# Performance work log

Measured on AMD Instinct MI355X. Metric: run time of the kernel, lower is better.

Reference implementation:

```python
import jax, jax.numpy as jnp
import numpy as np

ALPHA = 0.2  # LeakyReLU negative slope
NEG_INF = -9e15


def _gat_layer(Wh, adj, a, concat):
    """One GraphAttentionLayer given pre-projected Wh [B,N,F].
    Algebraic split of the concat attention: e[b,i,j] = lrelu(Wh[i]@a1 + Wh[j]@a2),
    identical math to matmul(cat(Wh_i, Wh_j), a)."""
    F_ = Wh.shape[-1]
    f1 = Wh @ a[:F_, 0]   # [B,N]
    f2 = Wh @ a[F_:, 0]   # [B,N]
    e = jax.nn.leaky_relu(f1[:, :, None] + f2[:, None, :], negative_slope=ALPHA)  # [B,N,N]
    e = jnp.where(adj > 0, e, NEG_INF)
    att = jax.nn.softmax(e, axis=-1)            # dropout omitted (eval mode)
    h_prime = jnp.einsum('bij,bjf->bif', att, Wh)
    return jax.nn.elu(h_prime) if concat else h_prime


def setup_inputs() -> dict:
    key = jax.random.key(0)
    ks = jax.random.split(key, 9)
    B, N, Fin, H, nH, Fout = 4, 2048, 512, 128, 4, 256
    x = jax.random.normal(ks[0], (B, N, Fin), dtype=jnp.float32)
    adj = jax.random.randint(ks[1], (B, N, N), 0, 2, dtype=jnp.int32)
    mask = jnp.ones((B, N), dtype=jnp.float32)
    s = 0.05
    W_heads = jax.random.normal(ks[2], (nH, Fin, H), dtype=jnp.float32) * s
    a_heads = jax.random.normal(ks[3], (nH, 2 * H, 1), dtype=jnp.float32) * s
    W_out = jax.random.normal(ks[4], (nH * H, Fout), dtype=jnp.float32) * s
    a_out = jax.random.normal(ks[5], (2 * Fout, 1), dtype=jnp.float32) * s
    W_pool = jax.random.normal(ks[6], (Fout, Fout), dtype=jnp.float32) * s
    b_pool = jax.random.normal(ks[7], (Fout,), dtype=jnp.float32) * s
    return {"x": x, "adj": adj, "mask": mask, "W_heads": W_heads, "a_heads": a_heads,
            "W_out": W_out, "a_out": a_out, "W_pool": W_pool, "b_pool": b_pool}


def reference(x, adj, mask, W_heads, a_heads, W_out, a_out, W_pool, b_pool):
    # multi-head GAT layer, heads concatenated (dropout = identity in eval)
    heads = [_gat_layer(x @ W_heads[h], adj, a_heads[h], concat=True)
             for h in range(W_heads.shape[0])]
    xcat = jnp.concatenate(heads, axis=-1)                 # [B,N,nH*H]
    x_out = _gat_layer(xcat @ W_out, adj, a_out, concat=False)  # [B,N,Fout]
    x_out = x_out * mask[:, :, None]
    pooled = x_out.sum(axis=1) / (mask.sum(axis=1, keepdims=True) + 1e-10)
    graph_embedding = jax.nn.relu(pooled @ W_pool + b_pool)
    return graph_embedding, x_out
```

## Files before the change

kernel.cpp:

```cpp
#include <hip/hip_runtime.h>

typedef unsigned short u16;
typedef __attribute__((ext_vector_type(8))) short s8v;
typedef __attribute__((ext_vector_type(8))) unsigned short us8;
typedef __attribute__((ext_vector_type(4))) float f4v;

#define L2E 1.4426950408889634f

typedef __attribute__((address_space(1))) void gvoid_t;
typedef __attribute__((address_space(3))) void lvoid_t;

__device__ __forceinline__ u16 f2bf(float f) {
  unsigned u = __builtin_bit_cast(unsigned, f);
  return (u16)((u + 0x7FFFu + ((u >> 16) & 1u)) >> 16);
}
__device__ __forceinline__ float bf2f(u16 h) {
  return __builtin_bit_cast(float, ((unsigned)h) << 16);
}
__device__ __forceinline__ f4v mfma16(s8v a, s8v b, f4v c) {
  return __builtin_amdgcn_mfma_f32_16x16x32_bf16(a, b, c, 0, 0, 0);
}
__device__ __forceinline__ float exp2fast(float x) {
#if __has_builtin(__builtin_amdgcn_exp2f)
  return __builtin_amdgcn_exp2f(x);
#else
  return exp2f(x);
#endif
}
__device__ __forceinline__ void stage16(const u16* g, u16* lds_arr, int slot) {
#if __has_builtin(__builtin_amdgcn_global_load_lds)
  __builtin_amdgcn_global_load_lds((gvoid_t*)(g),
      (lvoid_t*)(lds_arr + (size_t)(slot & ~63) * 8), 16, 0, 0);
#else
  *(us8*)(lds_arr + (size_t)slot * 8) = *(const us8*)g;
#endif
}

__global__ __launch_bounds__(256) void prep_x(const float* __restrict__ x,
                                              u16* __restrict__ xb) {
  int i = (blockIdx.x * 256 + threadIdx.x) * 8;
  float4 v0 = *(const float4*)(x + i);
  float4 v1 = *(const float4*)(x + i + 4);
  us8 o;
  o[0] = f2bf(v0.x); o[1] = f2bf(v0.y); o[2] = f2bf(v0.z); o[3] = f2bf(v0.w);
  o[4] = f2bf(v1.x); o[5] = f2bf(v1.y); o[6] = f2bf(v1.z); o[7] = f2bf(v1.w);
  *(us8*)(xb + i) = o;
}

__global__ __launch_bounds__(256) void prep_wall(const float* __restrict__ W,
                                                 u16* __restrict__ Wt) {
  int idx = blockIdx.x * 256 + threadIdx.x;
  int h = idx >> 16, k = (idx >> 7) & 511, f = idx & 127;
  Wt[(size_t)(h * 128 + f) * 512 + k] = f2bf(W[idx]);
}
__global__ __launch_bounds__(256) void prep_wout(const float* __restrict__ W,
                                                 u16* __restrict__ Wt) {
  int idx = blockIdx.x * 256 + threadIdx.x;
  int k = idx >> 8, c = idx & 255;
  Wt[(size_t)c * 512 + k] = f2bf(W[idx]);
}
__global__ __launch_bounds__(256) void prep_adj(const int* __restrict__ adj,
                                                unsigned* __restrict__ adjw) {
  int chunk = blockIdx.x * 4 + (threadIdx.x >> 6);
  int l = threadIdx.x & 63;
  int v = adj[(size_t)chunk * 64 + l];
  unsigned long long m = __ballot(v != 0);
  if (l == 0) {
    ((uint2*)adjw)[chunk] = make_uint2((unsigned)m, (unsigned)(m >> 32));
  }
}

__global__ __launch_bounds__(256) void gemm_bf16(const u16* __restrict__ A,
                                                 const u16* __restrict__ Bt,
                                                 u16* __restrict__ Ct, int CO) {
  const int K = 512, N = 2048;
  int m0 = blockIdx.x * 128;
  int n0 = blockIdx.y * 128;
  int t = threadIdx.x;
  int w = t >> 6, l = t & 63, lr = l & 15, lq = l >> 4;
  int wr = w >> 1, wc = w & 1;
  __shared__ u16 As[2][128 * 32];
  __shared__ u16 Bs[2][128 * 32];
  f4v zero4 = {0.f, 0.f, 0.f, 0.f};
  f4v acc[4][4];
#pragma unroll
  for (int i = 0; i < 4; ++i)
#pragma unroll
    for (int j = 0; j < 4; ++j) acc[i][j] = zero4;

  auto stage = [&](int buf, int kt) {
    int k0 = kt * 32;
    int row = t >> 2, ch = t & 3;
    int q = (ch ^ ((row >> 1) & 3)) * 8;
    stage16(A + (size_t)(m0 + row) * K + k0 + q, As[buf], t);
    stage16(Bt + (size_t)(n0 + row) * K + k0 + q, Bs[buf], t);
    int s2 = t + 256;
    row = s2 >> 2; ch = s2 & 3;
    q = (ch ^ ((row >> 1) & 3)) * 8;
    stage16(A + (size_t)(m0 + row) * K + k0 + q, As[buf], s2);
    stage16(Bt + (size_t)(n0 + row) * K + k0 + q, Bs[buf], s2);
  };
  stage(0, 0);
  int swz = (lq ^ ((lr >> 1) & 3)) * 8;
  for (int kt = 0; kt < 16; ++kt) {
    __syncthreads();
    if (kt < 15) stage((kt + 1) & 1, kt + 1);
    const u16* as = As[kt & 1];
    const u16* bs = Bs[kt & 1];
    s8v af[4], bfr[4];
#pragma unroll
    for (int rf = 0; rf < 4; ++rf)
      af[rf] = *(const s8v*)&as[(wr * 64 + rf * 16 + lr) * 32 + swz];
#pragma unroll
    for (int nf = 0; nf < 4; ++nf)
      bfr[nf] = *(const s8v*)&bs[(wc * 64 + nf * 16 + lr) * 32 + swz];
#pragma unroll
    for (int rf = 0; rf < 4; ++rf)
#pragma unroll
      for (int nf = 0; nf < 4; ++nf)
        acc[rf][nf] = mfma16(af[rf], bfr[nf], acc[rf][nf]);
  }
  int bidx = m0 >> 11;
  int nr0 = m0 & 2047;
#pragma unroll
  for (int rf = 0; rf < 4; ++rf) {
#pragma unroll
    for (int nf = 0; nf < 4; ++nf) {
      int col = n0 + wc * 64 + nf * 16 + lr;
      int nr = nr0 + wr * 64 + rf * 16 + lq * 4;
      f4v a = acc[rf][nf];
      ushort4 v = make_ushort4(f2bf(a[0]), f2bf(a[1]), f2bf(a[2]), f2bf(a[3]));
      *(ushort4*)&Ct[((size_t)bidx * CO + col) * N + nr] = v;
    }
  }
}

__global__ __launch_bounds__(256) void fkern(const u16* __restrict__ Wht,
                                             const float* __restrict__ a,
                                             float* __restrict__ f1L,
                                             float* __restrict__ f2L, int COLS,
                                             int F) {
  const int N = 2048;
  int h = blockIdx.z, b = blockIdx.y;
  int nl = threadIdx.x & 63, fc = threadIdx.x >> 6;
  int n = blockIdx.x * 64 + nl;
  int F4 = F >> 2;
  const u16* colp = Wht + ((size_t)(b * COLS + h * F + fc * F4)) * N + n;
  const float* ah = a + h * 2 * F + fc * F4;
  float a1 = 0.f, a2 = 0.f;
  for (int c = 0; c < F4; ++c) {
    float v = bf2f(colp[(size_t)c * N]);
    a1 = fmaf(v, ah[c], a1);
    a2 = fmaf(v, ah[F + c], a2);
  }
  __shared__ float r1[4][64], r2[4][64];
  r1[fc][nl] = a1;
  r2[fc][nl] = a2;
  __syncthreads();
  if (fc == 0) {
    float s1 = r1[0][nl] + r1[1][nl] + r1[2][nl] + r1[3][nl];
    float s2 = r2[0][nl] + r2[1][nl] + r2[2][nl] + r2[3][nl];
    f1L[(size_t)(h * 4 + b) * N + n] = s1 * L2E;
    f2L[(size_t)(h * 4 + b) * N + n] = s2 * L2E;
  }
}

__global__ __launch_bounds__(256) void fmax_kern(const float* __restrict__ f2L,
                                                 float* __restrict__ f2m) {
  int row = blockIdx.x;
  const float* p = f2L + (size_t)row * 2048;
  int t = threadIdx.x;
  float v = -__builtin_inff();
  for (int k = 0; k < 8; ++k) v = fmaxf(v, p[t + k * 256]);
#pragma unroll
  for (int d = 1; d < 64; d <<= 1) v = fmaxf(v, __shfl_xor(v, d));
  __shared__ float wm[4];
  if ((t & 63) == 0) wm[t >> 6] = v;
  __syncthreads();
  if (t == 0) f2m[row] = fmaxf(fmaxf(wm[0], wm[1]), fmaxf(wm[2], wm[3]));
}

template <int CT, int WR, bool ELU>
__global__ __launch_bounds__(256, 2) void attn_kernel(
    const u16* __restrict__ Wht, const float* __restrict__ f1L,
    const float* __restrict__ f2L, const float* __restrict__ f2max,
    const unsigned* __restrict__ adjw, const float* __restrict__ mask,
    void* __restrict__ outp) {
  const int N = 2048;
  constexpr int WC = 4 / WR;
  constexpr int NF = 8 / WC;
  constexpr int NCH = CT / 128;
  constexpr int ROWS = WR * 16;
  constexpr int NT = 2048 / ROWS;
  constexpr int FHD = (CT == 512) ? 1 : 0;
  int kb = blockIdx.x;
  int x = kb & 7, g = kb >> 3;
  int p = x + 8 * (g / NT);
  int it = g % NT;
  int b = p / NCH, ch = p % NCH;
  int i0 = it * ROWS, col0 = ch * 128;
  int fh = FHD ? ch : 0;
  int t = threadIdx.x;
  int w = t >> 6, l = t & 63, lr = l & 15, lq = l >> 4;
  int wc = w & (WC - 1), wrs = w / WC;

  __shared__ u16 Vs[2][128 * 64];
  __shared__ unsigned adjs[ROWS * 65];
  __shared__ float f2s[2048];

  const float* f1p = f1L + (size_t)(fh * 4 + b) * N + i0;
  const float* f2p = f2L + (size_t)(fh * 4 + b) * N;
  float f2m = f2max[fh * 4 + b];
  float f1v = f1p[wrs * 16 + lr];
  float su = f1v + f2m;
  float M = fmaxf(su, 0.2f * su);
  float c1 = f1v - M;
  float c2 = 0.2f * f1v - M;
  const u16* vbase = Wht + (size_t)(b * CT + col0) * 2048;

  for (int i = t; i < ROWS * 64; i += 256) {
    int row = i >> 6, wd = i & 63;
    adjs[row * 65 + wd] = adjw[(size_t)(b * N + i0 + row) * 64 + wd];
  }
  for (int i = t; i < 2048; i += 256) f2s[i] = f2p[i];

  auto stage = [&](int buf, int kt) {
    int k0 = kt * 64;
#pragma unroll
    for (int j2 = 0; j2 < 4; ++j2) {
      int s = j2 * 256 + t;
      int c = s >> 3, q = s & 7;
      stage16(vbase + (size_t)c * 2048 + k0 + (q ^ (c & 7)) * 8, Vs[buf], s);
    }
  };
  stage(0, 0);

  f4v zero4 = {0.f, 0.f, 0.f, 0.f};
  f4v acc[NF], accs = zero4;
#pragma unroll
  for (int j = 0; j < NF; ++j) acc[j] = zero4;
  s8v ones;
#pragma unroll
  for (int i = 0; i < 8; ++i) ones[i] = (short)0x3F80;

  for (int kt = 0; kt < 32; ++kt) {
    __syncthreads();
    if (kt < 31) stage((kt + 1) & 1, kt + 1);
    const u16* vs = Vs[kt & 1];
#pragma unroll
    for (int kk = 0; kk < 2; ++kk) {
      int jt = kt * 2 + kk;
      s8v vf[NF];
#pragma unroll
      for (int nf = 0; nf < NF; ++nf) {
        int c = wc * 64 + nf * 16 + lr;
        int chn = (kk * 4 + lq) ^ (lr & 7);
        vf[nf] = *(const s8v*)&vs[c * 64 + chn * 8];
      }
      float4 fa = *(const float4*)&f2s[jt * 32 + lq * 8];
      float4 fb = *(const float4*)&f2s[jt * 32 + lq * 8 + 4];
      float f2c[8] = {fa.x, fa.y, fa.z, fa.w, fb.x, fb.y, fb.z, fb.w};
      unsigned aw = adjs[(wrs * 16 + lr) * 65 + jt];
      union { s8v v; unsigned u[4]; } pk;
#pragma unroll
      for (int ep = 0; ep < 4; ++ep) {
        float t1 = c1 + f2c[2 * ep];
        float t2 = fmaf(0.2f, f2c[2 * ep], c2);
        float p0 = exp2fast(fmaxf(t1, t2));
        p0 = ((aw >> (lq * 8 + 2 * ep)) & 1u) ? p0 : 0.f;
        float t3 = c1 + f2c[2 * ep + 1];
        float t4 = fmaf(0.2f, f2c[2 * ep + 1], c2);
        float p1 = exp2fast(fmaxf(t3, t4));
        p1 = ((aw >> (lq * 8 + 2 * ep + 1)) & 1u) ? p1 : 0.f;
        asm("v_cvt_pk_bf16_f32 %0, %1, %2"
            : "=v"(pk.u[ep]) : "v"(p0), "v"(p1));
      }
      s8v pa = pk.v;
      accs = mfma16(pa, ones, accs);
#pragma unroll
      for (int nf = 0; nf < NF; ++nf)
        acc[nf] = mfma16(pa, vf[nf], acc[nf]);
    }
  }
  f4v i4;
#pragma unroll
  for (int r = 0; r < 4; ++r) i4[r] = 1.f / fmaxf(accs[r], 1e-30f);
  int rowb = i0 + wrs * 16 + lq * 4;
#pragma unroll
  for (int nf = 0; nf < NF; ++nf) {
    int col = col0 + wc * 64 + nf * 16 + lr;
#pragma unroll
    for (int r = 0; r < 4; ++r) {
      float v = acc[nf][r] * i4[r];
      size_t ob = (size_t)(b * N + rowb + r) * CT + col;
      if constexpr (ELU) {
        v = v > 0.f ? v : exp2fast(v * L2E) - 1.f;
        ((u16*)outp)[ob] = f2bf(v);
      } else {
        ((float*)outp)[ob] = v * mask[b * N + rowb + r];
      }
    }
  }
}

__global__ __launch_bounds__(256) void pool1(const float* __restrict__ xout,
                                             const float* __restrict__ mask,
                                             float* __restrict__ pool,
                                             float* __restrict__ den) {
  int b = blockIdx.x >> 6, s = blockIdx.x & 63;
  int c = threadIdx.x;
  int n0 = s * 32;
  float acc = 0.f;
  for (int r = 0; r < 32; ++r)
    acc += xout[((size_t)(b * 2048 + n0 + r)) * 256 + c];
  atomicAdd(&pool[b * 256 + c], acc);
  if (c == 0) {
    float ms = 0.f;
    for (int r = 0; r < 32; ++r) ms += mask[b * 2048 + n0 + r];
    atomicAdd(&den[b], ms);
  }
}
__global__ __launch_bounds__(256) void pool2(const float* __restrict__ pool,
                                             const float* __restrict__ den,
                                             const float* __restrict__ Wp,
                                             const float* __restrict__ bp,
                                             float* __restrict__ out) {
  int b = blockIdx.x, f = threadIdx.x;
  __shared__ float pv[256];
  float inv = 1.f / (den[b] + 1e-10f);
  pv[f] = pool[b * 256 + f] * inv;
  __syncthreads();
  float acc = bp[f];
  for (int c = 0; c < 256; ++c) acc = fmaf(pv[c], Wp[c * 256 + f], acc);
  out[b * 256 + f] = fmaxf(acc, 0.f);
}

extern "C" void kernel_launch(void* const* d_in, const int* in_sizes, int n_in,
                              void* d_out, int out_size, void* d_ws,
                              size_t ws_size, hipStream_t stream) {
  (void)in_sizes; (void)n_in; (void)out_size; (void)ws_size;
  const float* x = (const float*)d_in[0];
  const int* adj = (const int*)d_in[1];
  const float* mask = (const float*)d_in[2];
  const float* Whds = (const float*)d_in[3];
  const float* ahds = (const float*)d_in[4];
  const float* Wout = (const float*)d_in[5];
  const float* aout = (const float*)d_in[6];
  const float* Wpool = (const float*)d_in[7];
  const float* bpool = (const float*)d_in[8];
  float* out = (float*)d_out;

  char* ws = (char*)d_ws;
  size_t off = 0;
  auto take = [&](size_t n) {
    char* p = ws + off;
    off += (n + 255) & ~(size_t)255;
    return p;
  };
  u16* xb = (u16*)take(8192ull * 512 * 2);
  u16* Wta = (u16*)take(512ull * 512 * 2);
  u16* Wto = (u16*)take(256ull * 512 * 2);
  unsigned* adjw = (unsigned*)take(4ull * 2048 * 64 * 4);
  u16* Wht = (u16*)take(4ull * 512 * 2048 * 2);
  float* f1a = (float*)take(4ull * 4 * 2048 * 4);
  float* f2a = (float*)take(4ull * 4 * 2048 * 4);
  u16* xcat = (u16*)take(8192ull * 512 * 2);
  u16* Wh2t = (u16*)take(4ull * 256 * 2048 * 2);
  float* f1b = (float*)take(4ull * 2048 * 4);
  float* f2b = (float*)take(4ull * 2048 * 4);
  float* f2ma = (float*)take(16 * 4);
  float* f2mb = (float*)take(4 * 4);
  float* pool = (float*)take(1024 * 4);
  float* den = (float*)take(256);

  prep_x<<<2048, 256, 0, stream>>>(x, xb);
  prep_wall<<<1024, 256, 0, stream>>>(Whds, Wta);
  prep_wout<<<512, 256, 0, stream>>>(Wout, Wto);
  prep_adj<<<65536, 256, 0, stream>>>(adj, adjw);
  gemm_bf16<<<dim3(64, 4), 256, 0, stream>>>(xb, Wta, Wht, 512);
  fkern<<<dim3(32, 4, 4), 256, 0, stream>>>(Wht, ahds, f1a, f2a, 512, 128);
  fmax_kern<<<16, 256, 0, stream>>>(f2a, f2ma);
  attn_kernel<512, 4, true><<<512, 256, 0, stream>>>(Wht, f1a, f2a, f2ma,
                                                     adjw, nullptr, xcat);
  gemm_bf16<<<dim3(64, 2), 256, 0, stream>>>(xcat, Wto, Wh2t, 256);
  fkern<<<dim3(32, 4, 1), 256, 0, stream>>>(Wh2t, aout, f1b, f2b, 256, 256);
  fmax_kern<<<4, 256, 0, stream>>>(f2b, f2mb);
  attn_kernel<256, 2, false><<<512, 256, 0, stream>>>(Wh2t, f1b, f2b, f2mb,
                                                      adjw, mask, out + 1024);
  hipMemsetAsync(pool, 0, 4096 + 256, stream);
  pool1<<<256, 256, 0, stream>>>(out + 1024, mask, pool, den);
  pool2<<<4, 256, 0, stream>>>(pool, den, Wpool, bpool, out);
}
```

Before: 174.4 us.

## Repack V into MFMA fragment order and load directly from global

Adds a repack kernel that lays out the projected features in per-lane MFMA B-fragment order. The attention kernel then reads V fragments straight from global/L2 with coalesced 16-byte loads, dropping the double-buffered LDS staging and the barrier in every k-step. This frees LDS and removes synchronisation. The cost is two extra repack passes and a larger workspace. Each attention block now relies on L2 for reuse of V across row tiles, and global-load latency is no longer hidden by explicit prefetch.

```diff
diff --git a/kernel.cpp b/kernel.cpp
--- a/kernel.cpp
+++ b/kernel.cpp
@@ -135,6 +135,23 @@
   }
 }
 
+__global__ __launch_bounds__(256) void repack_v(const u16* __restrict__ Wht,
+                                                u16* __restrict__ Vf,
+                                                int COLS) {
+  int s = blockIdx.x * 256 + threadIdx.x;
+  int l = s & 63;
+  int lr = l & 15, lq = l >> 4;
+  int nf = (s >> 6) & 7;
+  int jt = (s >> 9) & 63;
+  int pnl = s >> 15;
+  int nch = COLS >> 7;
+  int b = pnl / nch, ch = pnl % nch;
+  int c = ch * 128 + nf * 16 + lr;
+  int j = jt * 32 + lq * 8;
+  *(us8*)(Vf + (size_t)s * 8) =
+      *(const us8*)(Wht + ((size_t)(b * COLS + c)) * 2048 + j);
+}
+
 __global__ __launch_bounds__(256) void fkern(const u16* __restrict__ Wht,
                                              const float* __restrict__ a,
                                              float* __restrict__ f1L,
@@ -182,7 +199,7 @@
 
 template <int CT, int WR, bool ELU>
 __global__ __launch_bounds__(256, 2) void attn_kernel(
-    const u16* __restrict__ Wht, const float* __restrict__ f1L,
+    const u16* __restrict__ Vf, const float* __restrict__ f1L,
     const float* __restrict__ f2L, const float* __restrict__ f2max,
     const unsigned* __restrict__ adjw, const float* __restrict__ mask,
     void* __restrict__ outp) {
@@ -204,7 +221,6 @@
   int w = t >> 6, l = t & 63, lr = l & 15, lq = l >> 4;
   int wc = w & (WC - 1), wrs = w / WC;
 
-  __shared__ u16 Vs[2][128 * 64];
   __shared__ unsigned adjs[ROWS * 65];
   __shared__ float f2s[2048];
 
@@ -216,24 +232,14 @@
   float M = fmaxf(su, 0.2f * su);
   float c1 = f1v - M;
   float c2 = 0.2f * f1v - M;
-  const u16* vbase = Wht + (size_t)(b * CT + col0) * 2048;
+  const u16* vpan = Vf + ((size_t)p * 64) * 4096;
 
   for (int i = t; i < ROWS * 64; i += 256) {
     int row = i >> 6, wd = i & 63;
     adjs[row * 65 + wd] = adjw[(size_t)(b * N + i0 + row) * 64 + wd];
   }
   for (int i = t; i < 2048; i += 256) f2s[i] = f2p[i];
-
-  auto stage = [&](int buf, int kt) {
-    int k0 = kt * 64;
-#pragma unroll
-    for (int j2 = 0; j2 < 4; ++j2) {
-      int s = j2 * 256 + t;
-      int c = s >> 3, q = s & 7;
-      stage16(vbase + (size_t)c * 2048 + k0 + (q ^ (c & 7)) * 8, Vs[buf], s);
-    }
-  };
-  stage(0, 0);
+  __syncthreads();
 
   f4v zero4 = {0.f, 0.f, 0.f, 0.f};
   f4v acc[NF], accs = zero4;
@@ -243,44 +249,35 @@
 #pragma unroll
   for (int i = 0; i < 8; ++i) ones[i] = (short)0x3F80;
 
-  for (int kt = 0; kt < 32; ++kt) {
-    __syncthreads();
-    if (kt < 31) stage((kt + 1) & 1, kt + 1);
-    const u16* vs = Vs[kt & 1];
-#pragma unroll
-    for (int kk = 0; kk < 2; ++kk) {
-      int jt = kt * 2 + kk;
-      s8v vf[NF];
-#pragma unroll
-      for (int nf = 0; nf < NF; ++nf) {
-        int c = wc * 64 + nf * 16 + lr;
-        int chn = (kk * 4 + lq) ^ (lr & 7);
-        vf[nf] = *(const s8v*)&vs[c * 64 + chn * 8];
-      }
-      float4 fa = *(const float4*)&f2s[jt * 32 + lq * 8];
-      float4 fb = *(const float4*)&f2s[jt * 32 + lq * 8 + 4];
-      float f2c[8] = {fa.x, fa.y, fa.z, fa.w, fb.x, fb.y, fb.z, fb.w};
-      unsigned aw = adjs[(wrs * 16 + lr) * 65 + jt];
-      union { s8v v; unsigned u[4]; } pk;
-#pragma unroll
-      for (int ep = 0; ep < 4; ++ep) {
-        float t1 = c1 + f2c[2 * ep];
-        float t2 = fmaf(0.2f, f2c[2 * ep], c2);
-        float p0 = exp2fast(fmaxf(t1, t2));
-        p0 = ((aw >> (lq * 8 + 2 * ep)) & 1u) ? p0 : 0.f;
-        float t3 = c1 + f2c[2 * ep + 1];
-        float t4 = fmaf(0.2f, f2c[2 * ep + 1], c2);
-        float p1 = exp2fast(fmaxf(t3, t4));
-        p1 = ((aw >> (lq * 8 + 2 * ep + 1)) & 1u) ? p1 : 0.f;
-        asm("v_cvt_pk_bf16_f32 %0, %1, %2"
-            : "=v"(pk.u[ep]) : "v"(p0), "v"(p1));
-      }
-      s8v pa = pk.v;
-      accs = mfma16(pa, ones, accs);
-#pragma unroll
-      for (int nf = 0; nf < NF; ++nf)
-        acc[nf] = mfma16(pa, vf[nf], acc[nf]);
+  for (int jt = 0; jt < 64; ++jt) {
+    const u16* vb = vpan + (size_t)jt * 4096;
+    s8v vf[NF];
+#pragma unroll
+    for (int nf = 0; nf < NF; ++nf)
+      vf[nf] = *(const s8v*)&vb[(size_t)((wc * 4 + nf) * 64 + l) * 8];
+    float4 fa = *(const float4*)&f2s[jt * 32 + lq * 8];
+    float4 fb = *(const float4*)&f2s[jt * 32 + lq * 8 + 4];
+    float f2c[8] = {fa.x, fa.y, fa.z, fa.w, fb.x, fb.y, fb.z, fb.w};
+    unsigned aw = adjs[(wrs * 16 + lr) * 65 + jt];
+    union { s8v v; unsigned u[4]; } pk;
+#pragma unroll
+    for (int ep = 0; ep < 4; ++ep) {
+      float t1 = c1 + f2c[2 * ep];
+      float t2 = fmaf(0.2f, f2c[2 * ep], c2);
+      float p0 = exp2fast(fmaxf(t1, t2));
+      p0 = ((aw >> (lq * 8 + 2 * ep)) & 1u) ? p0 : 0.f;
+      float t3 = c1 + f2c[2 * ep + 1];
+      float t4 = fmaf(0.2f, f2c[2 * ep + 1], c2);
+      float p1 = exp2fast(fmaxf(t3, t4));
+      p1 = ((aw >> (lq * 8 + 2 * ep + 1)) & 1u) ? p1 : 0.f;
+      asm("v_cvt_pk_bf16_f32 %0, %1, %2"
+          : "=v"(pk.u[ep]) : "v"(p0), "v"(p1));
     }
+    s8v pa = pk.v;
+    accs = mfma16(pa, ones, accs);
+#pragma unroll
+    for (int nf = 0; nf < NF; ++nf)
+      acc[nf] = mfma16(pa, vf[nf], acc[nf]);
   }
   f4v i4;
 #pragma unroll
@@ -362,10 +359,12 @@
   u16* Wto = (u16*)take(256ull * 512 * 2);
   unsigned* adjw = (unsigned*)take(4ull * 2048 * 64 * 4);
   u16* Wht = (u16*)take(4ull * 512 * 2048 * 2);
+  u16* Vf1 = (u16*)take(4ull * 512 * 2048 * 2);
   float* f1a = (float*)take(4ull * 4 * 2048 * 4);
   float* f2a = (float*)take(4ull * 4 * 2048 * 4);
   u16* xcat = (u16*)take(8192ull * 512 * 2);
   u16* Wh2t = (u16*)take(4ull * 256 * 2048 * 2);
+  u16* Vf2 = (u16*)take(4ull * 256 * 2048 * 2);
   float* f1b = (float*)take(4ull * 2048 * 4);
   float* f2b = (float*)take(4ull * 2048 * 4);
   float* f2ma = (float*)take(16 * 4);
@@ -378,14 +377,16 @@
   prep_wout<<<512, 256, 0, stream>>>(Wout, Wto);
   prep_adj<<<65536, 256, 0, stream>>>(adj, adjw);
   gemm_bf16<<<dim3(64, 4), 256, 0, stream>>>(xb, Wta, Wht, 512);
+  repack_v<<<2048, 256, 0, stream>>>(Wht, Vf1, 512);
   fkern<<<dim3(32, 4, 4), 256, 0, stream>>>(Wht, ahds, f1a, f2a, 512, 128);
   fmax_kern<<<16, 256, 0, stream>>>(f2a, f2ma);
-  attn_kernel<512, 4, true><<<512, 256, 0, stream>>>(Wht, f1a, f2a, f2ma,
+  attn_kernel<512, 4, true><<<512, 256, 0, stream>>>(Vf1, f1a, f2a, f2ma,
                                                      adjw, nullptr, xcat);
   gemm_bf16<<<dim3(64, 2), 256, 0, stream>>>(xcat, Wto, Wh2t, 256);
+  repack_v<<<1024, 256, 0, stream>>>(Wh2t, Vf2, 256);
   fkern<<<dim3(32, 4, 1), 256, 0, stream>>>(Wh2t, aout, f1b, f2b, 256, 256);
   fmax_kern<<<4, 256, 0, stream>>>(f2b, f2mb);
-  attn_kernel<256, 2, false><<<512, 256, 0, stream>>>(Wh2t, f1b, f2b, f2mb,
+  attn_kernel<256, 2, false><<<512, 256, 0, stream>>>(Vf2, f1b, f2b, f2mb,
                                                       adjw, mask, out + 1024);
   hipMemsetAsync(pool, 0, 4096 + 256, stream);
   pool1<<<256, 256, 0, stream>>>(out + 1024, mask, pool, den);
```

Result: slower. 267.1 us (+53.2%).
